# Performance work log

Hardware: AMD Instinct MI355X
Metric: run time of the kernel (lower is better)

The kernel has to match this reference:

```python
import jax, jax.numpy as jnp
import numpy as np

MARGIN = 0.2
W_HARD = 1.0
W_SOFT = 0.0
NORMALIZE = True
PD_EPS = 1e-6  # torch F.pairwise_distance eps used inside TripletMarginLoss


def setup_inputs() -> dict:
    key = jax.random.key(0)
    k1, k2, k3 = jax.random.split(key, 3)
    N, D = 8192, 128
    z = jax.random.normal(k1, (N, D), dtype=jnp.float32)
    labels = jax.random.randint(k2, (N,), 0, 16, dtype=jnp.int32)
    subjects = jax.random.randint(k3, (N,), 0, 32, dtype=jnp.int32)
    return {"z": z, "labels": labels, "subjects": subjects}


def _batch_hard(z, pos_mask, neg_mask, margin):
    # pairwise euclidean distances (cdist p=2); mining indices are ints, so
    # stop_gradient keeps vjp clean (matches torch: argmax/argmin detach).
    sq = jnp.sum(z * z, axis=1)
    d2 = sq[:, None] + sq[None, :] - 2.0 * (z @ z.T)
    dist = jax.lax.stop_gradient(jnp.sqrt(jnp.maximum(d2, 0.0)))
    inf = jnp.asarray(jnp.inf, dist.dtype)
    p_idx = jnp.argmax(jnp.where(pos_mask, dist, -inf), axis=1)  # hardest positive
    n_idx = jnp.argmin(jnp.where(neg_mask, dist, inf), axis=1)   # hardest negative
    valid = jnp.any(pos_mask, axis=1) & jnp.any(neg_mask, axis=1)
    a, p, n = z, z[p_idx], z[n_idx]
    d_ap = jnp.sqrt(jnp.sum((a - p + PD_EPS) ** 2, axis=1))
    d_an = jnp.sqrt(jnp.sum((a - n + PD_EPS) ** 2, axis=1))
    per = jnp.maximum(d_ap - d_an + margin, 0.0)
    cnt = jnp.sum(valid)
    loss = jnp.sum(per * valid) / jnp.maximum(cnt, 1).astype(per.dtype)
    return jnp.where(cnt > 0, loss, 0.0)


def reference(z, labels, subjects):
    if NORMALIZE:
        z = z / jnp.maximum(jnp.linalg.norm(z, axis=1, keepdims=True), 1e-12)
    N = z.shape[0]
    same_class = labels[:, None] == labels[None, :]
    same_subj = subjects[:, None] == subjects[None, :]
    not_eye = ~jnp.eye(N, dtype=bool)
    loss = 0.0
    denom = 0.0
    if W_HARD != 0:
        pos_hard = same_class & ~same_subj & not_eye
        neg_hard = ~same_class & same_subj & not_eye
        loss = loss + W_HARD * _batch_hard(z, pos_hard, neg_hard, MARGIN)
        denom += abs(W_HARD)
    if W_SOFT != 0:
        pos_soft = same_class & same_subj & not_eye
        neg_soft = ~same_class & ~same_subj & not_eye
        loss = loss + W_SOFT * _batch_hard(z, pos_soft, neg_soft, MARGIN)
        denom += abs(W_SOFT)
    return loss / max(denom, 1e-12)
```

## Files before the change

kernel.cpp:

```cpp
#include <hip/hip_runtime.h>
#include <math.h>

#define N 8192
#define D 128
#define MARGIN 0.2f
#define PD_EPS 1e-6f
#define NCHUNK 16
#define CHUNKJ (N / NCHUNK)

typedef __attribute__((ext_vector_type(8))) short bf16x8;
typedef __attribute__((ext_vector_type(4))) float f32x4;

__device__ __forceinline__ unsigned short f2bf(float f) {
    unsigned u = __float_as_uint(f);
    u += 0x7FFFu + ((u >> 16) & 1u);
    return (unsigned short)(u >> 16);
}
__device__ __forceinline__ unsigned umn(unsigned a, unsigned b) { return a < b ? a : b; }
__device__ __forceinline__ unsigned umx(unsigned a, unsigned b) { return a > b ? a : b; }

__global__ __launch_bounds__(256) void k_normalize(const float* __restrict__ z,
                                                   const int* __restrict__ labels,
                                                   const int* __restrict__ subjects,
                                                   unsigned short* __restrict__ znb,
                                                   float* __restrict__ invn,
                                                   int* __restrict__ meta) {
    int row  = blockIdx.x * 4 + (threadIdx.x >> 6);
    int lane = threadIdx.x & 63;
    float2 v = ((const float2*)(z + (size_t)row * D))[lane];
    float ss = v.x * v.x + v.y * v.y;
    #pragma unroll
    for (int m = 1; m < 64; m <<= 1) ss += __shfl_xor(ss, m, 64);
    float norm = fmaxf(sqrtf(ss), 1e-12f);
    float ox = v.x / norm, oy = v.y / norm;
    ushort2 b; b.x = f2bf(ox); b.y = f2bf(oy);
    ((ushort2*)(znb + (size_t)row * D))[lane] = b;
    if (lane == 0) {
        invn[row] = 1.0f / norm;
        meta[row] = labels[row] * 32 + subjects[row];
    }
}

__global__ __launch_bounds__(256, 2) void k_mine(const unsigned short* __restrict__ znb,
                                                 const int* __restrict__ meta,
                                                 unsigned* __restrict__ posk,
                                                 unsigned* __restrict__ negk) {
    const int wave = threadIdx.x >> 6;
    const int lane = threadIdx.x & 63;
    const int m    = lane & 15;
    const int quad = lane >> 4;
    const int iw   = (blockIdx.x * 4 + wave) * 64;
    const int jc   = blockIdx.y;
    const int jbase = jc * CHUNKJ;

    bf16x8 afrag[4][4];
    #pragma unroll
    for (int u = 0; u < 4; ++u)
        #pragma unroll
        for (int s = 0; s < 4; ++s)
            afrag[u][s] = *(const bf16x8*)(znb + (size_t)(iw + u * 16 + m) * D + s * 32 + quad * 8);

    int mi[16];
    #pragma unroll
    for (int u = 0; u < 4; ++u)
        #pragma unroll
        for (int r = 0; r < 4; ++r)
            mi[u * 4 + r] = meta[iw + u * 16 + quad * 4 + r];

    unsigned bp[16], bn[16];
    #pragma unroll
    for (int s = 0; s < 16; ++s) { bp[s] = 0xFFFFFFFFu; bn[s] = 0u; }

    for (int t = 0; t < CHUNKJ / 64; ++t) {
        const int jt = jbase + t * 64;

        f32x4 acc[4][4];
        #pragma unroll
        for (int u = 0; u < 4; ++u)
            #pragma unroll
            for (int v = 0; v < 4; ++v)
                acc[u][v] = (f32x4){0.f, 0.f, 0.f, 0.f};

        #pragma unroll
        for (int s = 0; s < 4; ++s) {
            bf16x8 bf[4];
            #pragma unroll
            for (int v = 0; v < 4; ++v)
                bf[v] = *(const bf16x8*)(znb + (size_t)(jt + v * 16 + m) * D + s * 32 + quad * 8);
            #pragma unroll
            for (int u = 0; u < 4; ++u)
                #pragma unroll
                for (int v = 0; v < 4; ++v)
                    acc[u][v] = __builtin_amdgcn_mfma_f32_16x16x32_bf16(afrag[u][s], bf[v], acc[u][v], 0, 0, 0);
        }

        #pragma unroll
        for (int v = 0; v < 4; ++v) {
            const int jv  = jt + v * 16 + m;
            const int mjv = meta[jv];
            #pragma unroll
            for (int u = 0; u < 4; ++u)
                #pragma unroll
                for (int r = 0; r < 4; ++r) {
                    float dot = acc[u][v][r];
                    unsigned key = (__float_as_uint(dot + 2.0f) & 0xFFFFE000u) | (unsigned)jv;
                    int x = mi[u * 4 + r] ^ mjv;
                    bool pos = (x != 0) && (x < 32);
                    bool neg = (x != 0) && ((x & 31) == 0);
                    bp[u * 4 + r] = umn(bp[u * 4 + r], pos ? key : 0xFFFFFFFFu);
                    bn[u * 4 + r] = umx(bn[u * 4 + r], neg ? key : 0u);
                }
        }
    }

    #pragma unroll
    for (int mm = 1; mm < 16; mm <<= 1)
        #pragma unroll
        for (int s = 0; s < 16; ++s) {
            bp[s] = umn(bp[s], (unsigned)__shfl_xor((int)bp[s], mm, 64));
            bn[s] = umx(bn[s], (unsigned)__shfl_xor((int)bn[s], mm, 64));
        }
    if (m == 0) {
        #pragma unroll
        for (int u = 0; u < 4; ++u)
            #pragma unroll
            for (int r = 0; r < 4; ++r) {
                int i = iw + u * 16 + quad * 4 + r;
                posk[(size_t)jc * N + i] = bp[u * 4 + r];
                negk[(size_t)jc * N + i] = bn[u * 4 + r];
            }
    }
}

__global__ __launch_bounds__(256) void k_final(const float* __restrict__ z,
                                               const float* __restrict__ invn,
                                               const unsigned* __restrict__ posk,
                                               const unsigned* __restrict__ negk,
                                               float* __restrict__ per, float* __restrict__ vld) {
    int row  = blockIdx.x * 4 + (threadIdx.x >> 6);
    int lane = threadIdx.x & 63;
    unsigned mp = 0xFFFFFFFFu, mn = 0u;
    #pragma unroll
    for (int c = 0; c < NCHUNK; ++c) {
        mp = umn(mp, posk[(size_t)c * N + row]);
        mn = umx(mn, negk[(size_t)c * N + row]);
    }
    bool valid = (mp != 0xFFFFFFFFu) && (mn != 0u);
    int pi = valid ? (int)(mp & 8191u) : 0;
    int ni = valid ? (int)(mn & 8191u) : 0;
    float ia = invn[row], ip = invn[pi], iq = invn[ni];
    float2 a = ((const float2*)(z + (size_t)row * D))[lane];
    float2 p = ((const float2*)(z + (size_t)pi  * D))[lane];
    float2 q = ((const float2*)(z + (size_t)ni  * D))[lane];
    float dx = a.x * ia - p.x * ip + PD_EPS, dy = a.y * ia - p.y * ip + PD_EPS;
    float sap = dx * dx + dy * dy;
    dx = a.x * ia - q.x * iq + PD_EPS; dy = a.y * ia - q.y * iq + PD_EPS;
    float san = dx * dx + dy * dy;
    #pragma unroll
    for (int m = 1; m < 64; m <<= 1) {
        sap += __shfl_xor(sap, m, 64);
        san += __shfl_xor(san, m, 64);
    }
    if (lane == 0) {
        float l = fmaxf(sqrtf(sap) - sqrtf(san) + MARGIN, 0.0f);
        per[row] = valid ? l : 0.0f;
        vld[row] = valid ? 1.0f : 0.0f;
    }
}

__global__ __launch_bounds__(256) void k_reduce(const float* __restrict__ per,
                                                const float* __restrict__ vld,
                                                float* __restrict__ out) {
    __shared__ float s1[256], s2[256];
    int t = threadIdx.x;
    float a = 0.f, b = 0.f;
    for (int i = t; i < N; i += 256) { a += per[i]; b += vld[i]; }
    s1[t] = a; s2[t] = b;
    __syncthreads();
    for (int w = 128; w > 0; w >>= 1) {
        if (t < w) { s1[t] += s1[t + w]; s2[t] += s2[t + w]; }
        __syncthreads();
    }
    if (t == 0) {
        float cnt = s2[0];
        out[0] = (cnt > 0.f) ? s1[0] / fmaxf(cnt, 1.f) : 0.f;
    }
}

extern "C" void kernel_launch(void* const* d_in, const int* in_sizes, int n_in,
                              void* d_out, int out_size, void* d_ws, size_t ws_size,
                              hipStream_t stream) {
    const float* z        = (const float*)d_in[0];
    const int*   labels   = (const int*)d_in[1];
    const int*   subjects = (const int*)d_in[2];
    float* out = (float*)d_out;

    char* ws = (char*)d_ws;
    unsigned short* znb = (unsigned short*)(ws);
    float*    invn = (float*)   (ws + 2097152);
    int*      meta = (int*)     (ws + 2129920);
    unsigned* posk = (unsigned*)(ws + 2162688);
    unsigned* negk = (unsigned*)(ws + 2686976);
    float*    per  = (float*)   (ws + 3211264);
    float*    vld  = (float*)   (ws + 3244032);

    k_normalize<<<dim3(N / 4), dim3(256), 0, stream>>>(z, labels, subjects, znb, invn, meta);
    k_mine<<<dim3(32, NCHUNK), dim3(256), 0, stream>>>(znb, meta, posk, negk);
    k_final<<<dim3(N / 4), dim3(256), 0, stream>>>(z, invn, posk, negk, per, vld);
    k_reduce<<<dim3(1), dim3(256), 0, stream>>>(per, vld, out);
}
```

Baseline: 116.9 us.

## Bucket rows by label and subject so mining only scans matching groups

```diff
diff --git a/kernel.cpp b/kernel.cpp
--- a/kernel.cpp
+++ b/kernel.cpp
@@ -5,8 +5,15 @@
 #define D 128
 #define MARGIN 0.2f
 #define PD_EPS 1e-6f
-#define NCHUNK 16
-#define CHUNKJ (N / NCHUNK)
+
+#define NLAB 16
+#define NSUB 32
+#define MAXPADL (N + NLAB * 64)
+#define MAXPADS (N + NSUB * 64)
+#define MAXWL 144
+#define MAXWS 160
+#define MAXW  (MAXWL + MAXWS)
+#define MINEBLOCKS ((MAXW + 3) / 4)
 
 typedef __attribute__((ext_vector_type(8))) short bf16x8;
 typedef __attribute__((ext_vector_type(4))) float f32x4;
@@ -19,12 +26,65 @@
 __device__ __forceinline__ unsigned umn(unsigned a, unsigned b) { return a < b ? a : b; }
 __device__ __forceinline__ unsigned umx(unsigned a, unsigned b) { return a > b ? a : b; }
 
+__global__ __launch_bounds__(256) void k_buckets(const int* __restrict__ labels,
+                                                 const int* __restrict__ subjects,
+                                                 int* __restrict__ metaL, int* __restrict__ permL,
+                                                 int* __restrict__ posL,
+                                                 int* __restrict__ metaS, int* __restrict__ permS,
+                                                 int* __restrict__ posS,
+                                                 int* __restrict__ wvA, int* __restrict__ wvJ,
+                                                 int* __restrict__ wvT) {
+    __shared__ int cL[NLAB], cS[NSUB], rL[NLAB], rS[NSUB], pbL[NLAB + 1], pbS[NSUB + 1];
+    const int t = threadIdx.x;
+    if (t < NLAB) { cL[t] = 0; rL[t] = 0; }
+    if (t < NSUB) { cS[t] = 0; rS[t] = 0; }
+    __syncthreads();
+    for (int i = t; i < N; i += 256) {
+        atomicAdd(&cL[labels[i]], 1);
+        atomicAdd(&cS[subjects[i]], 1);
+    }
+    __syncthreads();
+    if (t == 0) {
+        int a = 0;
+        for (int b = 0; b < NLAB; ++b) { pbL[b] = a; a += (cL[b] + 63) & ~63; }
+        pbL[NLAB] = a;
+        a = 0;
+        for (int b = 0; b < NSUB; ++b) { pbS[b] = a; a += (cS[b] + 63) & ~63; }
+        pbS[NSUB] = a;
+    }
+    __syncthreads();
+    for (int k = t; k < MAXPADL; k += 256) { metaL[k] = 1024; permL[k] = N; }
+    for (int k = t; k < MAXPADS; k += 256) { metaS[k] = 1024; permS[k] = N; }
+    __syncthreads();
+    for (int i = t; i < N; i += 256) {
+        int lab = labels[i], sub = subjects[i], me = lab * 32 + sub;
+        int kl = pbL[lab] + atomicAdd(&rL[lab], 1);
+        metaL[kl] = me; permL[kl] = i; posL[i] = kl;
+        int ks = pbS[sub] + atomicAdd(&rS[sub], 1);
+        metaS[ks] = me; permS[ks] = i; posS[i] = ks;
+    }
+    if (t == 0) {
+        int w = 0;
+        for (int b = 0; b < NLAB; ++b) {
+            int nt = (cL[b] + 63) >> 6;
+            for (int q = 0; q < nt; ++q) { wvA[w] = pbL[b] + q * 64; wvJ[w] = pbL[b]; wvT[w] = nt; ++w; }
+        }
+        for (; w < MAXWL; ++w) { wvA[w] = 0; wvJ[w] = 0; wvT[w] = 0; }
+        w = MAXWL;
+        for (int b = 0; b < NSUB; ++b) {
+            int nt = (cS[b] + 63) >> 6;
+            for (int q = 0; q < nt; ++q) { wvA[w] = pbS[b] + q * 64; wvJ[w] = pbS[b]; wvT[w] = nt; ++w; }
+        }
+        for (; w < MAXW; ++w) { wvA[w] = 0; wvJ[w] = 0; wvT[w] = 0; }
+    }
+}
+
 __global__ __launch_bounds__(256) void k_normalize(const float* __restrict__ z,
-                                                   const int* __restrict__ labels,
-                                                   const int* __restrict__ subjects,
-                                                   unsigned short* __restrict__ znb,
-                                                   float* __restrict__ invn,
-                                                   int* __restrict__ meta) {
+                                                   const int* __restrict__ posL,
+                                                   const int* __restrict__ posS,
+                                                   unsigned short* __restrict__ znbL,
+                                                   unsigned short* __restrict__ znbS,
+                                                   float* __restrict__ invn) {
     int row  = blockIdx.x * 4 + (threadIdx.x >> 6);
     int lane = threadIdx.x & 63;
     float2 v = ((const float2*)(z + (size_t)row * D))[lane];
@@ -32,47 +92,63 @@
     #pragma unroll
     for (int m = 1; m < 64; m <<= 1) ss += __shfl_xor(ss, m, 64);
     float norm = fmaxf(sqrtf(ss), 1e-12f);
-    float ox = v.x / norm, oy = v.y / norm;
-    ushort2 b; b.x = f2bf(ox); b.y = f2bf(oy);
-    ((ushort2*)(znb + (size_t)row * D))[lane] = b;
-    if (lane == 0) {
-        invn[row] = 1.0f / norm;
-        meta[row] = labels[row] * 32 + subjects[row];
-    }
-}
-
-__global__ __launch_bounds__(256, 2) void k_mine(const unsigned short* __restrict__ znb,
-                                                 const int* __restrict__ meta,
-                                                 unsigned* __restrict__ posk,
-                                                 unsigned* __restrict__ negk) {
+    ushort2 b; b.x = f2bf(v.x / norm); b.y = f2bf(v.y / norm);
+    int kl = posL[row], ks = posS[row];
+    ((ushort2*)(znbL + (size_t)kl * D))[lane] = b;
+    ((ushort2*)(znbS + (size_t)ks * D))[lane] = b;
+    if (lane == 0) invn[row] = 1.0f / norm;
+}
+
+__global__ __launch_bounds__(256) void k_mine(const unsigned short* __restrict__ znbL,
+                                              const unsigned short* __restrict__ znbS,
+                                              const int* __restrict__ metaL, const int* __restrict__ permL,
+                                              const int* __restrict__ metaS, const int* __restrict__ permS,
+                                              const int* __restrict__ wvA, const int* __restrict__ wvJ,
+                                              const int* __restrict__ wvT,
+                                              unsigned* __restrict__ posk, unsigned* __restrict__ negk) {
     const int wave = threadIdx.x >> 6;
     const int lane = threadIdx.x & 63;
+    const int w    = blockIdx.x * 4 + wave;
+    const int nt   = wvT[w];
+    if (nt == 0) return;
+    const bool isPos = (w < MAXWL);
+    const unsigned short* zb = isPos ? znbL : znbS;
+    const int* mt = isPos ? metaL : metaS;
+    const int* pm = isPos ? permL : permS;
+    const unsigned thr = isPos ? 31u : 1023u;
+    const unsigned inv = isPos ? 0u : 0xFFFFFFFFu;
+    const int ab = wvA[w];
+    const int jb = wvJ[w];
     const int m    = lane & 15;
     const int quad = lane >> 4;
-    const int iw   = (blockIdx.x * 4 + wave) * 64;
-    const int jc   = blockIdx.y;
-    const int jbase = jc * CHUNKJ;
 
     bf16x8 afrag[4][4];
     #pragma unroll
     for (int u = 0; u < 4; ++u)
         #pragma unroll
         for (int s = 0; s < 4; ++s)
-            afrag[u][s] = *(const bf16x8*)(znb + (size_t)(iw + u * 16 + m) * D + s * 32 + quad * 8);
+            afrag[u][s] = *(const bf16x8*)(zb + (size_t)(ab + u * 16 + m) * D + s * 32 + quad * 8);
 
     int mi[16];
     #pragma unroll
     for (int u = 0; u < 4; ++u)
         #pragma unroll
         for (int r = 0; r < 4; ++r)
-            mi[u * 4 + r] = meta[iw + u * 16 + quad * 4 + r];
-
-    unsigned bp[16], bn[16];
-    #pragma unroll
-    for (int s = 0; s < 16; ++s) { bp[s] = 0xFFFFFFFFu; bn[s] = 0u; }
-
-    for (int t = 0; t < CHUNKJ / 64; ++t) {
-        const int jt = jbase + t * 64;
+            mi[u * 4 + r] = mt[ab + u * 16 + quad * 4 + r];
+
+    unsigned best[16];
+    #pragma unroll
+    for (int s = 0; s < 16; ++s) best[s] = 0xFFFFFFFFu;
+
+    for (int t = 0; t < nt; ++t) {
+        const int jt = jb + t * 64;
+        int mjv[4], jov[4];
+        #pragma unroll
+        for (int v = 0; v < 4; ++v) {
+            int jr = jt + v * 16 + m;
+            mjv[v] = mt[jr];
+            jov[v] = pm[jr];
+        }
 
         f32x4 acc[4][4];
         #pragma unroll
@@ -86,7 +162,7 @@
             bf16x8 bf[4];
             #pragma unroll
             for (int v = 0; v < 4; ++v)
-                bf[v] = *(const bf16x8*)(znb + (size_t)(jt + v * 16 + m) * D + s * 32 + quad * 8);
+                bf[v] = *(const bf16x8*)(zb + (size_t)(jt + v * 16 + m) * D + s * 32 + quad * 8);
             #pragma unroll
             for (int u = 0; u < 4; ++u)
                 #pragma unroll
@@ -96,19 +172,15 @@
 
         #pragma unroll
         for (int v = 0; v < 4; ++v) {
-            const int jv  = jt + v * 16 + m;
-            const int mjv = meta[jv];
             #pragma unroll
             for (int u = 0; u < 4; ++u)
                 #pragma unroll
                 for (int r = 0; r < 4; ++r) {
                     float dot = acc[u][v][r];
-                    unsigned key = (__float_as_uint(dot + 2.0f) & 0xFFFFE000u) | (unsigned)jv;
-                    int x = mi[u * 4 + r] ^ mjv;
-                    bool pos = (x != 0) && (x < 32);
-                    bool neg = (x != 0) && ((x & 31) == 0);
-                    bp[u * 4 + r] = umn(bp[u * 4 + r], pos ? key : 0xFFFFFFFFu);
-                    bn[u * 4 + r] = umx(bn[u * 4 + r], neg ? key : 0u);
+                    unsigned key = (((__float_as_uint(dot + 2.0f)) & 0xFFFFE000u) | (unsigned)jov[v]) ^ inv;
+                    unsigned x = (unsigned)(mi[u * 4 + r] ^ mjv[v]);
+                    bool c = (x - 1u) < thr;
+                    best[u * 4 + r] = umn(best[u * 4 + r], c ? key : 0xFFFFFFFFu);
                 }
         }
     }
@@ -116,18 +188,17 @@
     #pragma unroll
     for (int mm = 1; mm < 16; mm <<= 1)
         #pragma unroll
-        for (int s = 0; s < 16; ++s) {
-            bp[s] = umn(bp[s], (unsigned)__shfl_xor((int)bp[s], mm, 64));
-            bn[s] = umx(bn[s], (unsigned)__shfl_xor((int)bn[s], mm, 64));
-        }
+        for (int s = 0; s < 16; ++s)
+            best[s] = umn(best[s], (unsigned)__shfl_xor((int)best[s], mm, 64));
+
     if (m == 0) {
+        unsigned* dst = isPos ? posk : negk;
         #pragma unroll
         for (int u = 0; u < 4; ++u)
             #pragma unroll
             for (int r = 0; r < 4; ++r) {
-                int i = iw + u * 16 + quad * 4 + r;
-                posk[(size_t)jc * N + i] = bp[u * 4 + r];
-                negk[(size_t)jc * N + i] = bn[u * 4 + r];
+                int orig = pm[ab + u * 16 + quad * 4 + r];
+                if (orig < N) dst[orig] = best[u * 4 + r] ^ inv;
             }
     }
 }
@@ -139,12 +210,8 @@
                                                float* __restrict__ per, float* __restrict__ vld) {
     int row  = blockIdx.x * 4 + (threadIdx.x >> 6);
     int lane = threadIdx.x & 63;
-    unsigned mp = 0xFFFFFFFFu, mn = 0u;
-    #pragma unroll
-    for (int c = 0; c < NCHUNK; ++c) {
-        mp = umn(mp, posk[(size_t)c * N + row]);
-        mn = umx(mn, negk[(size_t)c * N + row]);
-    }
+    unsigned mp = posk[row];
+    unsigned mn = negk[row];
     bool valid = (mp != 0xFFFFFFFFu) && (mn != 0u);
     int pi = valid ? (int)(mp & 8191u) : 0;
     int ni = valid ? (int)(mn & 8191u) : 0;
@@ -196,16 +263,29 @@
     float* out = (float*)d_out;
 
     char* ws = (char*)d_ws;
-    unsigned short* znb = (unsigned short*)(ws);
-    float*    invn = (float*)   (ws + 2097152);
-    int*      meta = (int*)     (ws + 2129920);
-    unsigned* posk = (unsigned*)(ws + 2162688);
-    unsigned* negk = (unsigned*)(ws + 2686976);
-    float*    per  = (float*)   (ws + 3211264);
-    float*    vld  = (float*)   (ws + 3244032);
-
-    k_normalize<<<dim3(N / 4), dim3(256), 0, stream>>>(z, labels, subjects, znb, invn, meta);
-    k_mine<<<dim3(32, NCHUNK), dim3(256), 0, stream>>>(znb, meta, posk, negk);
+    size_t o = 0;
+    unsigned short* znbL = (unsigned short*)(ws + o); o += (size_t)MAXPADL * D * 2;
+    unsigned short* znbS = (unsigned short*)(ws + o); o += (size_t)MAXPADS * D * 2;
+    float* invn = (float*)(ws + o); o += N * 4;
+    int* posL  = (int*)(ws + o); o += N * 4;
+    int* posS  = (int*)(ws + o); o += N * 4;
+    int* metaL = (int*)(ws + o); o += MAXPADL * 4;
+    int* permL = (int*)(ws + o); o += MAXPADL * 4;
+    int* metaS = (int*)(ws + o); o += MAXPADS * 4;
+    int* permS = (int*)(ws + o); o += MAXPADS * 4;
+    int* wvA   = (int*)(ws + o); o += 2048;
+    int* wvJ   = (int*)(ws + o); o += 2048;
+    int* wvT   = (int*)(ws + o); o += 2048;
+    unsigned* posk = (unsigned*)(ws + o); o += N * 4;
+    unsigned* negk = (unsigned*)(ws + o); o += N * 4;
+    float* per = (float*)(ws + o); o += N * 4;
+    float* vld = (float*)(ws + o); o += N * 4;
+
+    k_buckets<<<dim3(1), dim3(256), 0, stream>>>(labels, subjects, metaL, permL, posL,
+                                                 metaS, permS, posS, wvA, wvJ, wvT);
+    k_normalize<<<dim3(N / 4), dim3(256), 0, stream>>>(z, posL, posS, znbL, znbS, invn);
+    k_mine<<<dim3(MINEBLOCKS), dim3(256), 0, stream>>>(znbL, znbS, metaL, permL, metaS, permS,
+                                                       wvA, wvJ, wvT, posk, negk);
     k_final<<<dim3(N / 4), dim3(256), 0, stream>>>(z, invn, posk, negk, per, vld);
     k_reduce<<<dim3(1), dim3(256), 0, stream>>>(per, vld, out);
 }
```

After: 154.2 us. +32.0%, slower.
